# Kernel tuning notes

Hardware: AMD Instinct MI355X
Metric: run time of the kernel (lower is better)

The kernel has to match this reference:

```python
import jax, jax.numpy as jnp
import numpy as np

B, S, E = 8, 2048, 512
H = 8
LN_EPS = 1e-5


def _layer_norm(x, g, b):
    mu = jnp.mean(x, axis=-1, keepdims=True)
    var = jnp.mean((x - mu) ** 2, axis=-1, keepdims=True)
    return (x - mu) * jax.lax.rsqrt(var + LN_EPS) * g + b


def setup_inputs() -> dict:
    key = jax.random.key(0)
    ks = jax.random.split(key, 16)
    sc = 1.0 / np.sqrt(E)
    return {
        "q": jax.random.normal(ks[0], (B, S, E), jnp.float32),
        "k": jax.random.normal(ks[1], (B, S, E), jnp.float32),
        "trajectories": jax.random.normal(ks[2], (B, S, E), jnp.float32),
        "v_W": jax.random.normal(ks[3], (E, E), jnp.float32) * sc,
        "v_b": jnp.zeros((E,), jnp.float32),
        "out_W": jax.random.normal(ks[4], (E, E), jnp.float32) * sc,
        "out_b": jnp.zeros((E,), jnp.float32),
        "ln1_g": jnp.ones((E,), jnp.float32),
        "ln1_b": jnp.zeros((E,), jnp.float32),
        "ffn_w1": jax.random.normal(ks[5], (E, E), jnp.float32) * sc,
        "ffn_b1": jnp.zeros((E,), jnp.float32),
        "ffn_w2": jax.random.normal(ks[6], (E, E), jnp.float32) * sc,
        "ffn_b2": jnp.zeros((E,), jnp.float32),
        "ln2_g": jnp.ones((E,), jnp.float32),
        "ln2_b": jnp.zeros((E,), jnp.float32),
    }


def reference(q, k, trajectories, v_W, v_b, out_W, out_b, ln1_g, ln1_b,
              ffn_w1, ffn_b1, ffn_w2, ffn_b2, ln2_g, ln2_b):
    seq_len = q.shape[1]
    # V projection (v = k in the block's call). q_linear/k_linear are unused in the original forward.
    V = k @ v_W + v_b  # [B,S,E]; head split + per-head matmul + concat == single matmul

    # Multi-view trajectory similarity (TSMiniSimilarity), averaged over 4 views
    tn = trajectories / jnp.maximum(
        jnp.linalg.norm(trajectories, axis=-1, keepdims=True), 1e-12)
    c = jnp.einsum('bie,bje->bij', tn, tn)  # cosine similarity [B,S,S]
    aw = (jax.nn.sigmoid(c)
          + jax.nn.sigmoid(c * c)
          + jax.nn.sigmoid(jnp.exp(c - 1.0))
          + jax.nn.sigmoid(0.5 * c + 0.5)) * 0.25

    # First softmax over keys
    aw = jax.nn.softmax(aw, axis=-1)
    # ut_mask = triu(ones, diag=1); original fills where mask == 0 (lower triangle incl. diag)
    ut = jnp.triu(jnp.ones((seq_len, seq_len), dtype=bool), k=1)
    aw = jnp.where(ut, aw, -1e9)
    # Second softmax after masking
    aw = jax.nn.softmax(aw, axis=-1)

    attended = jnp.einsum('bij,bje->bie', aw, V)
    attn_out = attended @ out_W + out_b

    x = _layer_norm(q + attn_out, ln1_g, ln1_b)  # dropout is identity in eval
    h = jax.nn.relu(x @ ffn_w1 + ffn_b1) @ ffn_w2 + ffn_b2
    return _layer_norm(x + h, ln2_g, ln2_b)
```

## Files before the change

### kernel.cpp

```cpp
#include <hip/hip_runtime.h>

typedef __attribute__((ext_vector_type(8))) short s8v;
typedef __attribute__((ext_vector_type(4))) short s4v;
typedef __attribute__((ext_vector_type(4))) float f4v;

constexpr int SEQ = 2048;
constexpr int EMB = 512;
constexpr int BATCH = 8;
constexpr int BS = BATCH * SEQ;
constexpr int NCH = 32;

#define DEVINL __device__ __forceinline__

DEVINL float bf2f(short s) {
    union { unsigned u; float f; } v;
    v.u = ((unsigned)(unsigned short)s) << 16;
    return v.f;
}
DEVINL short f2bf(float f) {
    union { float f; unsigned u; } v; v.f = f;
    unsigned u = v.u;
    return (short)((u + 0x7FFFu + ((u >> 16) & 1u)) >> 16);
}
DEVINL f4v mfma16(s8v a, s8v b, f4v c) {
    return __builtin_amdgcn_mfma_f32_16x16x32_bf16(a, b, c, 0, 0, 0);
}
DEVINL s8v pack8(float4 a, float4 b) {
    s8v o;
    o[0] = f2bf(a.x); o[1] = f2bf(a.y); o[2] = f2bf(a.z); o[3] = f2bf(a.w);
    o[4] = f2bf(b.x); o[5] = f2bf(b.y); o[6] = f2bf(b.z); o[7] = f2bf(b.w);
    return o;
}
DEVINL void gload16(const short* g, short* l) {
    __builtin_amdgcn_global_load_lds(
        (const __attribute__((address_space(1))) void*)g,
        (__attribute__((address_space(3))) void*)l, 16, 0, 0);
}

__global__ __launch_bounds__(256) void prep_combo(
    const float* __restrict__ v_W, const float* __restrict__ out_W,
    const float* __restrict__ w1, const float* __restrict__ w2,
    const float* __restrict__ K, const float* __restrict__ v_b,
    const float* __restrict__ out_b,
    short* __restrict__ VWb, short* __restrict__ WoT,
    short* __restrict__ W1T, short* __restrict__ W2T,
    float* __restrict__ partial, float* __restrict__ bc) {
    __shared__ __attribute__((aligned(16))) char smem[4 * EMB * 4];
    const int blk = blockIdx.x;
    const int tid = threadIdx.x;

    if (blk < 128) {
        int i = blk * 256 + tid;
        const float* p = v_W + (size_t)i * 8;
        float4 a = *(const float4*)p;
        float4 b = *(const float4*)(p + 4);
        *(s8v*)(VWb + (size_t)i * 8) = pack8(a, b);
    } else if (blk < 320) {
        __shared__ short tile[64][72];
        int t = blk - 128;
        int sel = t >> 6;
        const float* W = (sel == 0) ? out_W : (sel == 1 ? w1 : w2);
        short* WT = (sel == 0) ? WoT : (sel == 1 ? W1T : W2T);
        int tileid = t & 63;
        int kt = (tileid >> 3) * 64, nt = (tileid & 7) * 64;
        int r = tid >> 4;
        int c4 = (tid & 15) * 4;
#pragma unroll
        for (int p = 0; p < 4; p++) {
            int row = p * 16 + r;
            float4 v = *(const float4*)(W + (size_t)(kt + row) * EMB + nt + c4);
            tile[row][c4 + 0] = f2bf(v.x);
            tile[row][c4 + 1] = f2bf(v.y);
            tile[row][c4 + 2] = f2bf(v.z);
            tile[row][c4 + 3] = f2bf(v.w);
        }
        __syncthreads();
        int kl = (tid & 7) * 8;
        int nl = tid >> 3;
#pragma unroll
        for (int h = 0; h < 2; h++) {
            int n = h * 32 + nl;
            s8v o;
#pragma unroll
            for (int e = 0; e < 8; e++) o[e] = tile[kl + e][n];
            *(s8v*)(WT + (size_t)(nt + n) * EMB + kt + kl) = o;
        }
    } else if (blk < 576) {
        float* sh = (float*)smem;
        int bb = blk - 320;
        int b = bb >> 5, c = bb & (NCH - 1);
        int g = tid >> 6, lane = tid & 63;
        int col8 = lane * 8;
        const float* base = K + ((size_t)b * SEQ + c * 64 + g * 16) * EMB + col8;
        float acc[8] = {};
        for (int it = 0; it < 16; it++) {
            float4 a = *(const float4*)(base + (size_t)it * EMB);
            float4 b2 = *(const float4*)(base + (size_t)it * EMB + 4);
            acc[0] += a.x; acc[1] += a.y; acc[2] += a.z; acc[3] += a.w;
            acc[4] += b2.x; acc[5] += b2.y; acc[6] += b2.z; acc[7] += b2.w;
        }
#pragma unroll
        for (int j = 0; j < 8; j++) sh[g * EMB + col8 + j] = acc[j];
        __syncthreads();
        if (g == 0) {
#pragma unroll
            for (int j = 0; j < 8; j++) {
                int e = col8 + j;
                partial[((size_t)b * NCH + c) * EMB + e] =
                    sh[e] + sh[EMB + e] + sh[2 * EMB + e] + sh[3 * EMB + e];
            }
        }
    } else {
        float* sh = (float*)smem;
        int bb = blk - 576;
        int nl = tid & 31, ms = tid >> 5;
        int n = bb * 32 + nl;
        float acc = 0.f;
#pragma unroll 8
        for (int mm = 0; mm < 64; mm++) {
            int m = ms * 64 + mm;
            acc = fmaf(v_b[m], out_W[(size_t)m * EMB + n], acc);
        }
        sh[tid] = acc;
        __syncthreads();
        if (tid < 32) {
            float s = 0.f;
#pragma unroll
            for (int j = 0; j < 8; j++) s += sh[j * 32 + tid];
            bc[bb * 32 + tid] = s + out_b[bb * 32 + tid];
        }
    }
}

__global__ __launch_bounds__(256, 2) void mid_combo(
    const short* __restrict__ VWb, const short* __restrict__ WoT,
    short* __restrict__ WcT,
    const float* __restrict__ K, const float* __restrict__ partial,
    short* __restrict__ SK) {
    __shared__ __attribute__((aligned(16))) short lds[2][16384];
    __shared__ float wsum[4][EMB];

    if (blockIdx.x < 16) {
        const int bid = blockIdx.x;
        const int wg = (bid & 7) * 2 + (bid >> 3);
        const int mt = wg >> 2, nt = wg & 3;
        const int mbase = mt * 128, nbase = nt * 128;
        const int tid = threadIdx.x;
        const int w = tid >> 6, lane = tid & 63;
        const int lr = lane & 15, kg = lane >> 4;
        const int wr = w >> 1, wc = w & 1;

        const short* gA[4];
        const short* gB[4];
        short* lA[4];
        short* lB[4];
#pragma unroll
        for (int inst = 0; inst < 4; inst++) {
            int U = inst * 256 + w * 64 + lane;
            int row = U >> 3, cu = U & 7;
            int csrc = cu ^ (row & 7);
            gA[inst] = VWb + (size_t)(mbase + row) * EMB + csrc * 8;
            gB[inst] = WoT + (size_t)(nbase + row) * EMB + csrc * 8;
            lA[inst] = &lds[0][(inst * 256 + w * 64) * 8];
            lB[inst] = &lds[0][8192 + (inst * 256 + w * 64) * 8];
        }
        int aoff[4][2], boff[4][2];
#pragma unroll
        for (int m = 0; m < 4; m++)
#pragma unroll
            for (int ks = 0; ks < 2; ks++) {
                int row = wr * 64 + m * 16 + lr;
                int cu = (ks * 4 + kg) ^ (row & 7);
                aoff[m][ks] = row * 64 + cu * 8;
            }
#pragma unroll
        for (int n = 0; n < 4; n++)
#pragma unroll
            for (int ks = 0; ks < 2; ks++) {
                int row = wc * 64 + n * 16 + lr;
                int cu = (ks * 4 + kg) ^ (row & 7);
                boff[n][ks] = 8192 + row * 64 + cu * 8;
            }
        auto stage = [&](int kt, int d) {
            int koff = kt * 64;
            int dd = d * 16384;
#pragma unroll
            for (int inst = 0; inst < 4; inst++)
                gload16(gA[inst] + koff, lA[inst] + dd);
#pragma unroll
            for (int inst = 0; inst < 4; inst++)
                gload16(gB[inst] + koff, lB[inst] + dd);
        };
        f4v acc[4][4] = {};
        stage(0, 0);
        int cur = 0;
        for (int kt = 0; kt < 8; kt++) {
            __syncthreads();
            if (kt < 7) stage(kt + 1, cur ^ 1);
            const short* base = &lds[cur][0];
            s8v afr[4][2], bfr[4][2];
#pragma unroll
            for (int m = 0; m < 4; m++)
#pragma unroll
                for (int ks = 0; ks < 2; ks++)
                    afr[m][ks] = *(const s8v*)(base + aoff[m][ks]);
#pragma unroll
            for (int n = 0; n < 4; n++)
#pragma unroll
                for (int ks = 0; ks < 2; ks++)
                    bfr[n][ks] = *(const s8v*)(base + boff[n][ks]);
#pragma unroll
            for (int ks = 0; ks < 2; ks++)
#pragma unroll
                for (int m = 0; m < 4; m++)
#pragma unroll
                    for (int n = 0; n < 4; n++)
                        acc[m][n] = mfma16(afr[m][ks], bfr[n][ks], acc[m][n]);
            cur ^= 1;
        }
#pragma unroll
        for (int m = 0; m < 4; m++)
#pragma unroll
            for (int n = 0; n < 4; n++) {
                int col = nbase + wc * 64 + n * 16 + lr;
                int row0 = mbase + wr * 64 + m * 16 + kg * 4;
                s4v o;
#pragma unroll
                for (int r = 0; r < 4; r++) o[r] = f2bf(acc[m][n][r]);
                *(s4v*)(WcT + (size_t)col * EMB + row0) = o;
            }
    } else {
        int bid = blockIdx.x - 16;
        int b = bid >> 5, c = bid & (NCH - 1);
        int g = threadIdx.x >> 6, lane = threadIdx.x & 63;
        int col8 = lane * 8;

        float off[8] = {}, alltot[8] = {};
        for (int cc = 0; cc < NCH; cc++) {
            const float* pp = partial + ((size_t)b * NCH + cc) * EMB + col8;
            float4 pa = *(const float4*)pp;
            float4 pb = *(const float4*)(pp + 4);
            float v[8] = {pa.x, pa.y, pa.z, pa.w, pb.x, pb.y, pb.z, pb.w};
#pragma unroll
            for (int j = 0; j < 8; j++) {
                alltot[j] += v[j];
                if (cc > c) off[j] += v[j];
            }
        }
        const float* base = K + ((size_t)b * SEQ + c * 64 + g * 16) * EMB + col8;
        {
            float acc[8] = {};
            for (int it = 0; it < 16; it++) {
                float4 a = *(const float4*)(base + (size_t)it * EMB);
                float4 bb = *(const float4*)(base + (size_t)it * EMB + 4);
                acc[0] += a.x; acc[1] += a.y; acc[2] += a.z; acc[3] += a.w;
                acc[4] += bb.x; acc[5] += bb.y; acc[6] += bb.z; acc[7] += bb.w;
            }
#pragma unroll
            for (int j = 0; j < 8; j++) wsum[g][col8 + j] = acc[j];
        }
        __syncthreads();
        float suf[8];
#pragma unroll
        for (int j = 0; j < 8; j++) {
            float s = off[j];
            for (int gg = g + 1; gg < 4; gg++) s += wsum[gg][col8 + j];
            suf[j] = s;
        }
        short* skbase = SK + ((size_t)b * SEQ + c * 64 + g * 16) * EMB + col8;
        for (int it = 15; it >= 0; it--) {
            int gi = c * 64 + g * 16 + it;
            float4 a = *(const float4*)(base + (size_t)it * EMB);
            float4 bb = *(const float4*)(base + (size_t)it * EMB + 4);
            s8v o;
            if (gi == SEQ - 1) {
                float inv = 1.0f / (float)SEQ;
#pragma unroll
                for (int j = 0; j < 8; j++) o[j] = f2bf(alltot[j] * inv);
            } else {
                float inv = __builtin_amdgcn_rcpf((float)(SEQ - 1 - gi));
#pragma unroll
                for (int j = 0; j < 8; j++) o[j] = f2bf(suf[j] * inv);
            }
            *(s8v*)(skbase + (size_t)it * EMB) = o;
            suf[0] += a.x; suf[1] += a.y; suf[2] += a.z; suf[3] += a.w;
            suf[4] += bb.x; suf[5] += bb.y; suf[6] += bb.z; suf[7] += bb.w;
        }
    }
}

template <int EPI>
__global__ __launch_bounds__(256, 2) void mgemm(
    const short* __restrict__ A, const short* __restrict__ B,
    const float* __restrict__ bias, short* __restrict__ C) {
    __shared__ __attribute__((aligned(16))) short lds[2][16384];

    const int nwg = gridDim.x;
    const int q = nwg >> 3;
    const int bid = blockIdx.x;
    const int wg = (bid & 7) * q + (bid >> 3);
    const int mt = wg >> 2, nt = wg & 3;
    const int mbase = mt * 128, nbase = nt * 128;

    const int tid = threadIdx.x;
    const int w = tid >> 6, lane = tid & 63;
    const int lr = lane & 15, kg = lane >> 4;
    const int wr = w >> 1, wc = w & 1;

    const short* gA[4];
    const short* gB[4];
    short* lA[4];
    short* lB[4];
#pragma unroll
    for (int inst = 0; inst < 4; inst++) {
        int U = inst * 256 + w * 64 + lane;
        int row = U >> 3, cu = U & 7;
        int csrc = cu ^ (row & 7);
        gA[inst] = A + (size_t)(mbase + row) * EMB + csrc * 8;
        gB[inst] = B + (size_t)(nbase + row) * EMB + csrc * 8;
        lA[inst] = &lds[0][(inst * 256 + w * 64) * 8];
        lB[inst] = &lds[0][8192 + (inst * 256 + w * 64) * 8];
    }

    int aoff[4][2], boff[4][2];
#pragma unroll
    for (int m = 0; m < 4; m++)
#pragma unroll
        for (int ks = 0; ks < 2; ks++) {
            int row = wr * 64 + m * 16 + lr;
            int cu = (ks * 4 + kg) ^ (row & 7);
            aoff[m][ks] = row * 64 + cu * 8;
        }
#pragma unroll
    for (int n = 0; n < 4; n++)
#pragma unroll
        for (int ks = 0; ks < 2; ks++) {
            int row = wc * 64 + n * 16 + lr;
            int cu = (ks * 4 + kg) ^ (row & 7);
            boff[n][ks] = 8192 + row * 64 + cu * 8;
        }

    auto stage = [&](int kt, int d) {
        int koff = kt * 64;
        int dd = d * 16384;
#pragma unroll
        for (int inst = 0; inst < 4; inst++)
            gload16(gA[inst] + koff, lA[inst] + dd);
#pragma unroll
        for (int inst = 0; inst < 4; inst++)
            gload16(gB[inst] + koff, lB[inst] + dd);
    };

    f4v acc[4][4] = {};
    stage(0, 0);
    int cur = 0;
    for (int kt = 0; kt < 8; kt++) {
        __syncthreads();
        if (kt < 7) stage(kt + 1, cur ^ 1);
        const short* base = &lds[cur][0];
        s8v afr[4][2], bfr[4][2];
#pragma unroll
        for (int m = 0; m < 4; m++)
#pragma unroll
            for (int ks = 0; ks < 2; ks++)
                afr[m][ks] = *(const s8v*)(base + aoff[m][ks]);
#pragma unroll
        for (int n = 0; n < 4; n++)
#pragma unroll
            for (int ks = 0; ks < 2; ks++)
                bfr[n][ks] = *(const s8v*)(base + boff[n][ks]);
#pragma unroll
        for (int ks = 0; ks < 2; ks++)
#pragma unroll
            for (int m = 0; m < 4; m++)
#pragma unroll
                for (int n = 0; n < 4; n++)
                    acc[m][n] = mfma16(afr[m][ks], bfr[n][ks], acc[m][n]);
        cur ^= 1;
    }

    float bcol[4];
#pragma unroll
    for (int n = 0; n < 4; n++) bcol[n] = bias[nbase + wc * 64 + n * 16 + lr];
#pragma unroll
    for (int m = 0; m < 4; m++)
#pragma unroll
        for (int n = 0; n < 4; n++) {
            int col = nbase + wc * 64 + n * 16 + lr;
#pragma unroll
            for (int r = 0; r < 4; r++) {
                int row = mbase + wr * 64 + m * 16 + kg * 4 + r;
                float v = acc[m][n][r] + bcol[n];
                if constexpr (EPI == 1) v = fmaxf(v, 0.f);
                C[(size_t)row * EMB + col] = f2bf(v);
            }
        }
}

__global__ __launch_bounds__(256) void ln1_kernel(
    const float* __restrict__ q, const short* __restrict__ VO2,
    const float* __restrict__ gam, const float* __restrict__ bet,
    short* __restrict__ Xbf) {
    int w = threadIdx.x >> 6, lane = threadIdx.x & 63;
    int row0 = blockIdx.x * 16 + w * 4;
    for (int it = 0; it < 4; it++) {
        size_t grow = row0 + it;
        const float* qp = q + grow * EMB + lane * 8;
        float4 qa = *(const float4*)qp;
        float4 qb = *(const float4*)(qp + 4);
        s8v ao = *(const s8v*)(VO2 + grow * EMB + lane * 8);
        float v[8];
        v[0] = qa.x + bf2f(ao[0]); v[1] = qa.y + bf2f(ao[1]);
        v[2] = qa.z + bf2f(ao[2]); v[3] = qa.w + bf2f(ao[3]);
        v[4] = qb.x + bf2f(ao[4]); v[5] = qb.y + bf2f(ao[5]);
        v[6] = qb.z + bf2f(ao[6]); v[7] = qb.w + bf2f(ao[7]);
        float s = 0.f, t = 0.f;
#pragma unroll
        for (int j = 0; j < 8; j++) { s += v[j]; t += v[j] * v[j]; }
#pragma unroll
        for (int m = 32; m >= 1; m >>= 1) {
            s += __shfl_xor(s, m);
            t += __shfl_xor(t, m);
        }
        float mean = s * (1.f / EMB);
        float var = t * (1.f / EMB) - mean * mean;
        float rstd = rsqrtf(var + 1e-5f);
        s8v xb;
#pragma unroll
        for (int j = 0; j < 8; j++) {
            int col = lane * 8 + j;
            xb[j] = f2bf((v[j] - mean) * rstd * gam[col] + bet[col]);
        }
        *(s8v*)(Xbf + grow * EMB + lane * 8) = xb;
    }
}

__global__ __launch_bounds__(256) void ln2_kernel(
    const short* __restrict__ Xbf, const short* __restrict__ Y,
    const float* __restrict__ gam, const float* __restrict__ bet,
    float* __restrict__ out) {
    int w = threadIdx.x >> 6, lane = threadIdx.x & 63;
    int row0 = blockIdx.x * 16 + w * 4;
    for (int it = 0; it < 4; it++) {
        size_t grow = row0 + it;
        s8v xv = *(const s8v*)(Xbf + grow * EMB + lane * 8);
        s8v yv = *(const s8v*)(Y + grow * EMB + lane * 8);
        float v[8];
#pragma unroll
        for (int j = 0; j < 8; j++) v[j] = bf2f(xv[j]) + bf2f(yv[j]);
        float s = 0.f, t = 0.f;
#pragma unroll
        for (int j = 0; j < 8; j++) { s += v[j]; t += v[j] * v[j]; }
#pragma unroll
        for (int m = 32; m >= 1; m >>= 1) {
            s += __shfl_xor(s, m);
            t += __shfl_xor(t, m);
        }
        float mean = s * (1.f / EMB);
        float var = t * (1.f / EMB) - mean * mean;
        float rstd = rsqrtf(var + 1e-5f);
        float xo[8];
#pragma unroll
        for (int j = 0; j < 8; j++) {
            int col = lane * 8 + j;
            xo[j] = (v[j] - mean) * rstd * gam[col] + bet[col];
        }
        float* op = out + grow * EMB + lane * 8;
        *(float4*)op = make_float4(xo[0], xo[1], xo[2], xo[3]);
        *(float4*)(op + 4) = make_float4(xo[4], xo[5], xo[6], xo[7]);
    }
}


extern "C" void kernel_launch(void* const* d_in, const int* in_sizes, int n_in,
                              void* d_out, int out_size, void* d_ws, size_t ws_size,
                              hipStream_t stream) {
    (void)in_sizes; (void)n_in; (void)out_size; (void)ws_size;
    const float* q     = (const float*)d_in[0];
    const float* k     = (const float*)d_in[1];
    const float* v_W   = (const float*)d_in[3];
    const float* v_b   = (const float*)d_in[4];
    const float* out_W = (const float*)d_in[5];
    const float* out_b = (const float*)d_in[6];
    const float* ln1_g = (const float*)d_in[7];
    const float* ln1_b = (const float*)d_in[8];
    const float* w1    = (const float*)d_in[9];
    const float* b1    = (const float*)d_in[10];
    const float* w2    = (const float*)d_in[11];
    const float* b2    = (const float*)d_in[12];
    const float* ln2_g = (const float*)d_in[13];
    const float* ln2_b = (const float*)d_in[14];

    char* ws = (char*)d_ws;
    const size_t MB = 1u << 20;
    short* SK   = (short*)(ws);
    short* VO2  = (short*)(ws + 16 * MB);
    short* Xbf  = (short*)(ws + 32 * MB);
    short* H1   = (short*)(ws + 48 * MB);
    short* Y    = (short*)(ws + 64 * MB);
    short* VWb  = (short*)(ws + 80 * MB);
    short* WoT  = VWb + 512 * 512;
    short* W1T  = WoT + 512 * 512;
    short* W2T  = W1T + 512 * 512;
    short* WcT  = W2T + 512 * 512;
    float* bc   = (float*)(WcT + 512 * 512);
    float* part = bc + EMB;

    prep_combo<<<592, 256, 0, stream>>>(v_W, out_W, w1, w2, k, v_b, out_b,
                                        VWb, WoT, W1T, W2T, part, bc);
    mid_combo<<<272, 256, 0, stream>>>(VWb, WoT, WcT, k, part, SK);
    mgemm<0><<<(BS / 128) * 4, 256, 0, stream>>>(SK, WcT, bc, VO2);
    ln1_kernel<<<BS / 16, 256, 0, stream>>>(q, VO2, ln1_g, ln1_b, Xbf);
    mgemm<1><<<(BS / 128) * 4, 256, 0, stream>>>(Xbf, W1T, b1, H1);
    mgemm<0><<<(BS / 128) * 4, 256, 0, stream>>>(H1, W2T, b2, Y);
    ln2_kernel<<<BS / 16, 256, 0, stream>>>(Xbf, Y, ln2_g, ln2_b, (float*)d_out);
}
```

Baseline: 90.53 us.

## Fuse residual add and LayerNorm into full-row GEMM epilogues

Adds a row-block GEMM (64 rows x full 512 columns, 512 threads) whose epilogue adds bias and residual, reduces row statistics across waves through LDS, and applies LayerNorm. It replaces the separate out-projection GEMM plus ln1 kernel and the FFN2 GEMM plus ln2 kernel. This removes two kernel launches and the bf16 intermediate write/read of VO2 and Y. In exchange each block is large and uses big LDS (about 74 KB), so occupancy drops, there are only 256 blocks, and the epilogue's residual loads and output stores are strided rather than vectorised.

```diff
diff --git a/kernel.cpp b/kernel.cpp
--- a/kernel.cpp
+++ b/kernel.cpp
@@ -289,8 +289,7 @@
     }
 }
 
-template <int EPI>
-__global__ __launch_bounds__(256, 2) void mgemm(
+__global__ __launch_bounds__(256, 2) void mgemm_relu(
     const short* __restrict__ A, const short* __restrict__ B,
     const float* __restrict__ bias, short* __restrict__ C) {
     __shared__ __attribute__((aligned(16))) short lds[2][16384];
@@ -390,85 +389,157 @@
 #pragma unroll
             for (int r = 0; r < 4; r++) {
                 int row = mbase + wr * 64 + m * 16 + kg * 4 + r;
-                float v = acc[m][n][r] + bcol[n];
-                if constexpr (EPI == 1) v = fmaxf(v, 0.f);
+                float v = fmaxf(acc[m][n][r] + bcol[n], 0.f);
                 C[(size_t)row * EMB + col] = f2bf(v);
             }
         }
 }
 
-__global__ __launch_bounds__(256) void ln1_kernel(
-    const float* __restrict__ q, const short* __restrict__ VO2,
+template <int EPI>
+__global__ __launch_bounds__(512) void rgemm(
+    const short* __restrict__ A, const short* __restrict__ B,
+    const float* __restrict__ bias, const void* __restrict__ resid,
     const float* __restrict__ gam, const float* __restrict__ bet,
-    short* __restrict__ Xbf) {
-    int w = threadIdx.x >> 6, lane = threadIdx.x & 63;
-    int row0 = blockIdx.x * 16 + w * 4;
-    for (int it = 0; it < 4; it++) {
-        size_t grow = row0 + it;
-        const float* qp = q + grow * EMB + lane * 8;
-        float4 qa = *(const float4*)qp;
-        float4 qb = *(const float4*)(qp + 4);
-        s8v ao = *(const s8v*)(VO2 + grow * EMB + lane * 8);
-        float v[8];
-        v[0] = qa.x + bf2f(ao[0]); v[1] = qa.y + bf2f(ao[1]);
-        v[2] = qa.z + bf2f(ao[2]); v[3] = qa.w + bf2f(ao[3]);
-        v[4] = qb.x + bf2f(ao[4]); v[5] = qb.y + bf2f(ao[5]);
-        v[6] = qb.z + bf2f(ao[6]); v[7] = qb.w + bf2f(ao[7]);
+    void* __restrict__ out) {
+    __shared__ __attribute__((aligned(16))) short lds[2][18432];
+    __shared__ float wsum[8][64], wsq[8][64];
+    __shared__ float mrow[64], rrow[64];
+
+    const int rb = blockIdx.x * 64;
+    const int tid = threadIdx.x;
+    const int w = tid >> 6, lane = tid & 63;
+    const int lr = lane & 15, kg = lane >> 4;
+
+    const short* gB[4];
+    short* lB[4];
+#pragma unroll
+    for (int inst = 0; inst < 4; inst++) {
+        int U = inst * 512 + tid;
+        int row = U >> 2, cu = U & 3;
+        int csrc = cu ^ ((row >> 1) & 3);
+        gB[inst] = B + (size_t)row * EMB + csrc * 8;
+        lB[inst] = &lds[0][2048 + U * 8];
+    }
+    const short* gA = nullptr;
+    short* lA = nullptr;
+    if (tid < 256) {
+        int row = tid >> 2, cu = tid & 3;
+        int csrc = cu ^ ((row >> 1) & 3);
+        gA = A + (size_t)(rb + row) * EMB + csrc * 8;
+        lA = &lds[0][tid * 8];
+    }
+
+    int aoff[4], boff[4];
+#pragma unroll
+    for (int m = 0; m < 4; m++) {
+        int row = m * 16 + lr;
+        int cu = kg ^ ((row >> 1) & 3);
+        aoff[m] = (row * 4 + cu) * 8;
+    }
+#pragma unroll
+    for (int n = 0; n < 4; n++) {
+        int row = w * 64 + n * 16 + lr;
+        int cu = kg ^ ((row >> 1) & 3);
+        boff[n] = 2048 + (row * 4 + cu) * 8;
+    }
+
+    auto stage = [&](int kt, int d) {
+        int koff = kt * 32;
+        int dd = d * 18432;
+#pragma unroll
+        for (int inst = 0; inst < 4; inst++)
+            gload16(gB[inst] + koff, lB[inst] + dd);
+        if (tid < 256) gload16(gA + koff, lA + dd);
+    };
+
+    f4v acc[4][4] = {};
+    stage(0, 0);
+    int cur = 0;
+    for (int kt = 0; kt < 16; kt++) {
+        __syncthreads();
+        if (kt < 15) stage(kt + 1, cur ^ 1);
+        const short* base = &lds[cur][0];
+        s8v af[4], bf[4];
+#pragma unroll
+        for (int m = 0; m < 4; m++) af[m] = *(const s8v*)(base + aoff[m]);
+#pragma unroll
+        for (int n = 0; n < 4; n++) bf[n] = *(const s8v*)(base + boff[n]);
+#pragma unroll
+        for (int m = 0; m < 4; m++)
+#pragma unroll
+            for (int n = 0; n < 4; n++)
+                acc[m][n] = mfma16(af[m], bf[n], acc[m][n]);
+        cur ^= 1;
+    }
+
+    float bcol[4], gcol[4], bet2[4];
+#pragma unroll
+    for (int n = 0; n < 4; n++) {
+        int col = w * 64 + n * 16 + lr;
+        bcol[n] = bias[col];
+        gcol[n] = gam[col];
+        bet2[n] = bet[col];
+    }
+    float sm[4][4] = {}, sq[4][4] = {};
+#pragma unroll
+    for (int m = 0; m < 4; m++)
+#pragma unroll
+        for (int n = 0; n < 4; n++) {
+            int col = w * 64 + n * 16 + lr;
+#pragma unroll
+            for (int r = 0; r < 4; r++) {
+                int row = m * 16 + kg * 4 + r;
+                size_t gidx = (size_t)(rb + row) * EMB + col;
+                float rv;
+                if constexpr (EPI == 0) rv = ((const float*)resid)[gidx];
+                else rv = bf2f(((const short*)resid)[gidx]);
+                float v = acc[m][n][r] + bcol[n] + rv;
+                acc[m][n][r] = v;
+                sm[m][r] += v;
+                sq[m][r] += v * v;
+            }
+        }
+#pragma unroll
+    for (int m = 0; m < 4; m++)
+#pragma unroll
+        for (int r = 0; r < 4; r++) {
+            float s = sm[m][r], t = sq[m][r];
+            s += __shfl_xor(s, 1); t += __shfl_xor(t, 1);
+            s += __shfl_xor(s, 2); t += __shfl_xor(t, 2);
+            s += __shfl_xor(s, 4); t += __shfl_xor(t, 4);
+            s += __shfl_xor(s, 8); t += __shfl_xor(t, 8);
+            if (lr == 0) {
+                int row = m * 16 + kg * 4 + r;
+                wsum[w][row] = s;
+                wsq[w][row] = t;
+            }
+        }
+    __syncthreads();
+    if (tid < 64) {
         float s = 0.f, t = 0.f;
 #pragma unroll
-        for (int j = 0; j < 8; j++) { s += v[j]; t += v[j] * v[j]; }
-#pragma unroll
-        for (int m = 32; m >= 1; m >>= 1) {
-            s += __shfl_xor(s, m);
-            t += __shfl_xor(t, m);
-        }
+        for (int ww = 0; ww < 8; ww++) { s += wsum[ww][tid]; t += wsq[ww][tid]; }
         float mean = s * (1.f / EMB);
         float var = t * (1.f / EMB) - mean * mean;
-        float rstd = rsqrtf(var + 1e-5f);
-        s8v xb;
-#pragma unroll
-        for (int j = 0; j < 8; j++) {
-            int col = lane * 8 + j;
-            xb[j] = f2bf((v[j] - mean) * rstd * gam[col] + bet[col]);
-        }
-        *(s8v*)(Xbf + grow * EMB + lane * 8) = xb;
-    }
-}
-
-__global__ __launch_bounds__(256) void ln2_kernel(
-    const short* __restrict__ Xbf, const short* __restrict__ Y,
-    const float* __restrict__ gam, const float* __restrict__ bet,
-    float* __restrict__ out) {
-    int w = threadIdx.x >> 6, lane = threadIdx.x & 63;
-    int row0 = blockIdx.x * 16 + w * 4;
-    for (int it = 0; it < 4; it++) {
-        size_t grow = row0 + it;
-        s8v xv = *(const s8v*)(Xbf + grow * EMB + lane * 8);
-        s8v yv = *(const s8v*)(Y + grow * EMB + lane * 8);
-        float v[8];
-#pragma unroll
-        for (int j = 0; j < 8; j++) v[j] = bf2f(xv[j]) + bf2f(yv[j]);
-        float s = 0.f, t = 0.f;
-#pragma unroll
-        for (int j = 0; j < 8; j++) { s += v[j]; t += v[j] * v[j]; }
-#pragma unroll
-        for (int m = 32; m >= 1; m >>= 1) {
-            s += __shfl_xor(s, m);
-            t += __shfl_xor(t, m);
-        }
-        float mean = s * (1.f / EMB);
-        float var = t * (1.f / EMB) - mean * mean;
-        float rstd = rsqrtf(var + 1e-5f);
-        float xo[8];
-#pragma unroll
-        for (int j = 0; j < 8; j++) {
-            int col = lane * 8 + j;
-            xo[j] = (v[j] - mean) * rstd * gam[col] + bet[col];
-        }
-        float* op = out + grow * EMB + lane * 8;
-        *(float4*)op = make_float4(xo[0], xo[1], xo[2], xo[3]);
-        *(float4*)(op + 4) = make_float4(xo[4], xo[5], xo[6], xo[7]);
-    }
+        mrow[tid] = mean;
+        rrow[tid] = rsqrtf(var + 1e-5f);
+    }
+    __syncthreads();
+#pragma unroll
+    for (int m = 0; m < 4; m++)
+#pragma unroll
+        for (int r = 0; r < 4; r++) {
+            int row = m * 16 + kg * 4 + r;
+            float mean = mrow[row], rstd = rrow[row];
+#pragma unroll
+            for (int n = 0; n < 4; n++) {
+                int col = w * 64 + n * 16 + lr;
+                size_t gidx = (size_t)(rb + row) * EMB + col;
+                float y = (acc[m][n][r] - mean) * rstd * gcol[n] + bet2[n];
+                if constexpr (EPI == 0) ((short*)out)[gidx] = f2bf(y);
+                else ((float*)out)[gidx] = y;
+            }
+        }
 }
 
 
@@ -494,11 +565,9 @@
     char* ws = (char*)d_ws;
     const size_t MB = 1u << 20;
     short* SK   = (short*)(ws);
-    short* VO2  = (short*)(ws + 16 * MB);
-    short* Xbf  = (short*)(ws + 32 * MB);
-    short* H1   = (short*)(ws + 48 * MB);
-    short* Y    = (short*)(ws + 64 * MB);
-    short* VWb  = (short*)(ws + 80 * MB);
+    short* Xbf  = (short*)(ws + 16 * MB);
+    short* H1   = (short*)(ws + 32 * MB);
+    short* VWb  = (short*)(ws + 48 * MB);
     short* WoT  = VWb + 512 * 512;
     short* W1T  = WoT + 512 * 512;
     short* W2T  = W1T + 512 * 512;
@@ -509,9 +578,8 @@
     prep_combo<<<592, 256, 0, stream>>>(v_W, out_W, w1, w2, k, v_b, out_b,
                                         VWb, WoT, W1T, W2T, part, bc);
     mid_combo<<<272, 256, 0, stream>>>(VWb, WoT, WcT, k, part, SK);
-    mgemm<0><<<(BS / 128) * 4, 256, 0, stream>>>(SK, WcT, bc, VO2);
-    ln1_kernel<<<BS / 16, 256, 0, stream>>>(q, VO2, ln1_g, ln1_b, Xbf);
-    mgemm<1><<<(BS / 128) * 4, 256, 0, stream>>>(Xbf, W1T, b1, H1);
-    mgemm<0><<<(BS / 128) * 4, 256, 0, stream>>>(H1, W2T, b2, Y);
-    ln2_kernel<<<BS / 16, 256, 0, stream>>>(Xbf, Y, ln2_g, ln2_b, (float*)d_out);
-}
+    rgemm<0><<<BS / 64, 512, 0, stream>>>(SK, WcT, bc, q, ln1_g, ln1_b, Xbf);
+    mgemm_relu<<<(BS / 128) * 4, 256, 0, stream>>>(Xbf, W1T, b1, H1);
+    rgemm<1><<<BS / 64, 512, 0, stream>>>(H1, W2T, b2, Xbf, ln2_g, ln2_b,
+                                          (float*)d_out);
+}
```

Result: slower. 97.14 us (+7.3%).
